# Kernel optimization log

Hardware: AMD Instinct MI355X
Metric: run time of the kernel (lower is better)

The kernel has to match this reference:

```python
import jax, jax.numpy as jnp
import numpy as np

N_HEAD = 16
SCALE = float(np.sqrt(1024 // N_HEAD))  # source multiplies by sqrt(head_dim) (faithful to bug)


def setup_inputs() -> dict:
    key = jax.random.key(0)
    ks = jax.random.split(key, 4)
    B, T, D = 4, 2048, 1024
    std = 1.0 / np.sqrt(D)
    return {
        "x": jax.random.normal(ks[0], (B, T, D), dtype=jnp.float32),
        "Wq": jax.random.normal(ks[1], (D, D), dtype=jnp.float32) * std,
        "bq": jnp.zeros((D,), dtype=jnp.float32),
        "Wk": jax.random.normal(ks[2], (D, D), dtype=jnp.float32) * std,
        "bk": jnp.zeros((D,), dtype=jnp.float32),
        "Wv": jax.random.normal(ks[3], (D, D), dtype=jnp.float32) * std,
        "bv": jnp.zeros((D,), dtype=jnp.float32),
    }


def reference(x, Wq, bq, Wk, bk, Wv, bv):
    B, T, D = x.shape
    H = N_HEAD
    hd = D // H
    # linear projections (torch Linear: x @ W^T + b)
    q = x @ Wq.T + bq
    k = x @ Wk.T + bk
    v = x @ Wv.T + bv
    # [B, H, T, hd]
    q = q.reshape(B, T, H, hd).transpose(0, 2, 1, 3)
    k = k.reshape(B, T, H, hd).transpose(0, 2, 1, 3)
    v = v.reshape(B, T, H, hd).transpose(0, 2, 1, 3)
    # scores [B, H, T, T]; note: source MULTIPLIES by sqrt(head_dim)
    att = jnp.einsum("bhqd,bhkd->bhqk", q, k) * SCALE
    causal = jnp.tril(jnp.ones((T, T), dtype=bool))
    att = jnp.where(causal, att, -jnp.inf)
    att = jax.nn.softmax(att, axis=-1)
    y = jnp.einsum("bhqk,bhkd->bhqd", att, v)
    return y.transpose(0, 2, 1, 3).reshape(B, T, D)
```

## Files before the change

kernel.cpp:

```cpp
#include <hip/hip_runtime.h>
#include <math.h>

#define TSEQ   2048
#define NBATCH 4
#define NHEAD  16
#define HDIM   64
#define DMODEL 1024
#define MROWS  (NBATCH * TSEQ)
#define QSCALE 11.541560327111707f

typedef float f32x4  __attribute__((ext_vector_type(4)));
typedef short bf16x8 __attribute__((ext_vector_type(8)));
typedef _Float16 f16x8 __attribute__((ext_vector_type(8)));

static __device__ __forceinline__ short f2bf(float f) {
    union { float f; unsigned u; } a; a.f = f;
    unsigned r = a.u + 0x7FFFu + ((a.u >> 16) & 1u);
    return (short)(r >> 16);
}
static __device__ __forceinline__ float bf2f(short s) {
    union { unsigned u; float f; } a; a.u = ((unsigned)(unsigned short)s) << 16;
    return a.f;
}
static __device__ __forceinline__ unsigned pkh(float a, float b) {
    union { _Float16 h[2]; unsigned u; } z;
    z.h[0] = (_Float16)a; z.h[1] = (_Float16)b;
    return z.u;
}

static __device__ __forceinline__ void async_copy16(void* lds, const void* g) {
    __builtin_amdgcn_global_load_lds(
        (const __attribute__((address_space(1))) void*)g,
        (__attribute__((address_space(3))) void*)lds, 16, 0, 0);
}

#define X_F4 (MROWS * DMODEL / 4)
#define W_F4 (DMODEL * DMODEL / 4)
__global__ __launch_bounds__(256) void split_all(
    const float* __restrict__ x,
    const float* __restrict__ wq, const float* __restrict__ wk,
    const float* __restrict__ wv,
    short* __restrict__ Xhi, short* __restrict__ Xlo,
    short* __restrict__ Whi, short* __restrict__ Wlo)
{
    int gid = blockIdx.x * 256 + threadIdx.x;
    const float* src; short* dh; short* dl; int off;
    if (gid < X_F4) {
        src = x; dh = Xhi; dl = Xlo; off = gid;
    } else {
        int r = gid - X_F4;
        int z = r >> 18;
        off = r & (W_F4 - 1);
        src = (z == 0) ? wq : (z == 1) ? wk : wv;
        dh = Whi + (size_t)z * DMODEL * DMODEL;
        dl = Wlo + (size_t)z * DMODEL * DMODEL;
    }
    float4 v = ((const float4*)src)[off];
    float f[4] = {v.x, v.y, v.z, v.w};
    short h[4], l[4];
    #pragma unroll
    for (int c = 0; c < 4; c++) {
        h[c] = f2bf(f[c]);
        l[c] = f2bf(f[c] - bf2f(h[c]));
    }
    *(float2*)(dh + (size_t)off * 4) = *(const float2*)h;
    *(float2*)(dl + (size_t)off * 4) = *(const float2*)l;
}

__global__ __launch_bounds__(256, 2) void qkv_gemm_mfma(
    const short* __restrict__ Xhi, const short* __restrict__ Xlo,
    const short* __restrict__ Wh3, const short* __restrict__ Wl3,
    const float* __restrict__ bq, const float* __restrict__ bk,
    const float* __restrict__ bv,
    short* __restrict__ Qhi, short* __restrict__ Qlo,
    short* __restrict__ Khi, short* __restrict__ Klo,
    _Float16* __restrict__ VgT)
{
    const int z = blockIdx.z;
    const bool dolo = (z != 2);
    const short* Wh = Wh3 + (size_t)z * DMODEL * DMODEL;
    const short* Wl = Wl3 + (size_t)z * DMODEL * DMODEL;
    const float* bias = (z == 0) ? bq : (z == 1) ? bk : bv;

    __shared__ __align__(16) short Ah[128 * 32];
    __shared__ __align__(16) short Al[128 * 32];
    __shared__ __align__(16) short Bh[128 * 32];
    __shared__ __align__(16) short Bl[128 * 32];

    const int tid  = threadIdx.x;
    const int w    = tid >> 6;
    const int lane = tid & 63;
    const int t    = lane & 15;
    const int quad = lane >> 4;
    const int wm   = w >> 1, wn = w & 1;

    const int orig = blockIdx.x + (blockIdx.y << 3);
    const int nw   = (orig & 7) * 64 + (orig >> 3);
    const int bm   = (nw >> 3) * 128;
    const int bn   = (nw & 7) * 128;

    const int r_local = lane >> 2;
    const int kq      = (lane & 3) ^ ((r_local >> 1) & 3);
    const int row0    = w * 32 + r_local;
    const int slotq   = (quad ^ ((t >> 1) & 3)) * 8;

    f32x4 acc[4][4];
    #pragma unroll
    for (int i = 0; i < 4; i++)
        #pragma unroll
        for (int j = 0; j < 4; j++) acc[i][j] = (f32x4){0.f, 0.f, 0.f, 0.f};

    for (int k0 = 0; k0 < DMODEL; k0 += 32) {
        __syncthreads();
        #pragma unroll
        for (int i = 0; i < 2; i++) {
            int row = row0 + i * 16;
            size_t ga = (size_t)(bm + row) * DMODEL + k0 + kq * 8;
            size_t gb = (size_t)(bn + row) * DMODEL + k0 + kq * 8;
            int ldst = (w * 32 + i * 16) * 32;
            async_copy16(&Ah[ldst], Xhi + ga);
            async_copy16(&Bh[ldst], Wh + gb);
            if (dolo) {
                async_copy16(&Al[ldst], Xlo + ga);
                async_copy16(&Bl[ldst], Wl + gb);
            }
        }
        __syncthreads();

        bf16x8 ah[4], al[4], bh[4], bl[4];
        #pragma unroll
        for (int mt = 0; mt < 4; mt++) {
            int off = (wm * 64 + mt * 16 + t) * 32 + slotq;
            ah[mt] = *(const bf16x8*)&Ah[off];
            if (dolo) al[mt] = *(const bf16x8*)&Al[off];
        }
        #pragma unroll
        for (int nt = 0; nt < 4; nt++) {
            int off = (wn * 64 + nt * 16 + t) * 32 + slotq;
            bh[nt] = *(const bf16x8*)&Bh[off];
            if (dolo) bl[nt] = *(const bf16x8*)&Bl[off];
        }
        #pragma unroll
        for (int mt = 0; mt < 4; mt++)
            #pragma unroll
            for (int nt = 0; nt < 4; nt++) {
                if (dolo) {
                    acc[mt][nt] = __builtin_amdgcn_mfma_f32_16x16x32_bf16(
                        al[mt], bh[nt], acc[mt][nt], 0, 0, 0);
                    acc[mt][nt] = __builtin_amdgcn_mfma_f32_16x16x32_bf16(
                        ah[mt], bl[nt], acc[mt][nt], 0, 0, 0);
                }
                acc[mt][nt] = __builtin_amdgcn_mfma_f32_16x16x32_bf16(
                    ah[mt], bh[nt], acc[mt][nt], 0, 0, 0);
            }
    }

    const float scale = (z == 0) ? QSCALE : 1.0f;
    const int n_base = bn + wn * 64;
    const int h_head = n_base >> 6;
    float bvs[4];
    #pragma unroll
    for (int nt = 0; nt < 4; nt++)
        bvs[nt] = bias[n_base + nt * 16 + t];

    #pragma unroll
    for (int mt = 0; mt < 4; mt++) {
        #pragma unroll
        for (int r = 0; r < 4; r++) {
            int m  = bm + wm * 64 + mt * 16 + quad * 4 + r;
            int b_ = m >> 11;
            int t_ = m & 2047;
            #pragma unroll
            for (int nt = 0; nt < 4; nt++) {
                int d = nt * 16 + t;
                float v = (acc[mt][nt][r] + bvs[nt]) * scale;
                if (z == 2) {
                    size_t idx = ((size_t)(b_ * NHEAD + h_head) * HDIM + d) * TSEQ + t_;
                    VgT[idx] = (_Float16)v;
                } else {
                    size_t idx = (((size_t)(b_ * NHEAD + h_head) * TSEQ + t_) << 6) + d;
                    short hb = f2bf(v);
                    short lb = f2bf(v - bf2f(hb));
                    if (z == 0) { Qhi[idx] = hb; Qlo[idx] = lb; }
                    else        { Khi[idx] = hb; Klo[idx] = lb; }
                }
            }
        }
    }
}

__global__ __launch_bounds__(256, 3) void attn_fwd(
    const short* __restrict__ Qhi, const short* __restrict__ Qlo,
    const short* __restrict__ Khi, const short* __restrict__ Klo,
    const _Float16* __restrict__ VgT,
    float* __restrict__ out)
{
    __shared__ __align__(16) short    Kh_lds[2][64 * 64];
    __shared__ __align__(16) short    Kl_lds[2][64 * 64];
    __shared__ __align__(16) _Float16 Vt_lds[2][64 * 64];

    const int tid  = threadIdx.x;

    const int l    = blockIdx.x;
    const int xcd  = l & 7;
    const int idx  = l >> 3;
    const int bh   = xcd * 8 + (idx & 7);
    const int qb   = 15 - (idx >> 3);

    const int b    = bh >> 4, h = bh & 15;
    const int w    = tid >> 6;
    const int lane = tid & 63;
    const int t    = lane & 15;
    const int quad = lane >> 4;

    const int rl      = w * 8 + (lane >> 3);
    const int chsw    = (lane & 7) ^ ((lane >> 3) & 7);
    const int ld_off  = (w * 8) * 64;

    const size_t kbase = (size_t)bh * TSEQ;
    const size_t vbase = (size_t)bh * HDIM;

    const int rs0 = ((0 * 4 + quad) ^ (t & 7)) * 8;
    const int rs1 = ((1 * 4 + quad) ^ (t & 7)) * 8;
    const int qsw = ((quad & 1) << 1) | (quad >> 1);
    const int rp0 = ((0 * 4 + qsw) ^ (t & 7)) * 8;
    const int rp1 = ((1 * 4 + qsw) ^ (t & 7)) * 8;
    const bool hi4 = (quad & 1);

    f16x8 ones;
    #pragma unroll
    for (int i = 0; i < 8; i++) ones[i] = (_Float16)1.0f;

    auto stage = [&](int kt, int bf) {
        #pragma unroll
        for (int i = 0; i < 2; i++) {
            int row = i * 32 + rl;
            const short* gk = Khi + (kbase + kt * 64 + row) * 64 + chsw * 8;
            async_copy16(&Kh_lds[bf][(i * 32) * 64 + ld_off], gk);
            const short* gl = Klo + (kbase + kt * 64 + row) * 64 + chsw * 8;
            async_copy16(&Kl_lds[bf][(i * 32) * 64 + ld_off], gl);
            const _Float16* gv = VgT + (vbase + row) * TSEQ + kt * 64 + chsw * 8;
            async_copy16(&Vt_lds[bf][(i * 32) * 64 + ld_off], gv);
        }
    };

    bf16x8 qh[2][2], ql[2][2];
    #pragma unroll
    for (int mt = 0; mt < 2; mt++) {
        size_t qrow = kbase + qb * 128 + w * 32 + mt * 16 + t;
        #pragma unroll
        for (int dh = 0; dh < 2; dh++) {
            qh[mt][dh] = *(const bf16x8*)(Qhi + qrow * 64 + dh * 32 + quad * 8);
            ql[mt][dh] = *(const bf16x8*)(Qlo + qrow * 64 + dh * 32 + quad * 8);
        }
    }

    f32x4 O[2][4], Ol[2];
    #pragma unroll
    for (int mt = 0; mt < 2; mt++) {
        Ol[mt] = (f32x4){0.f, 0.f, 0.f, 0.f};
        #pragma unroll
        for (int j = 0; j < 4; j++) O[mt][j] = (f32x4){0.f, 0.f, 0.f, 0.f};
    }
    float m_st[2];
    m_st[0] = -1e30f; m_st[1] = -1e30f;

    const int npair = qb + 1;

    #pragma unroll 1
    for (int p = 0; p < npair; p++) {
        __syncthreads();
        stage(2 * p, 0);
        stage(2 * p + 1, 1);
        __syncthreads();

        #pragma unroll
        for (int mt = 0; mt < 2; mt++) {
            f32x4 S[8];
            __builtin_amdgcn_s_setprio(1);
            #pragma unroll
            for (int c8 = 0; c8 < 8; c8++) {
                S[c8] = (f32x4){0.f, 0.f, 0.f, 0.f};
                const int bf = c8 >> 2;
                const int rowoff = ((c8 & 3) * 16 + t) * 64;
                {
                    bf16x8 kh = *(const bf16x8*)&Kh_lds[bf][rowoff + rs0];
                    bf16x8 kl = *(const bf16x8*)&Kl_lds[bf][rowoff + rs0];
                    S[c8] = __builtin_amdgcn_mfma_f32_16x16x32_bf16(kh, ql[mt][0], S[c8], 0, 0, 0);
                    S[c8] = __builtin_amdgcn_mfma_f32_16x16x32_bf16(kl, qh[mt][0], S[c8], 0, 0, 0);
                    S[c8] = __builtin_amdgcn_mfma_f32_16x16x32_bf16(kh, qh[mt][0], S[c8], 0, 0, 0);
                }
                {
                    bf16x8 kh = *(const bf16x8*)&Kh_lds[bf][rowoff + rs1];
                    bf16x8 kl = *(const bf16x8*)&Kl_lds[bf][rowoff + rs1];
                    S[c8] = __builtin_amdgcn_mfma_f32_16x16x32_bf16(kh, ql[mt][1], S[c8], 0, 0, 0);
                    S[c8] = __builtin_amdgcn_mfma_f32_16x16x32_bf16(kl, qh[mt][1], S[c8], 0, 0, 0);
                    S[c8] = __builtin_amdgcn_mfma_f32_16x16x32_bf16(kh, qh[mt][1], S[c8], 0, 0, 0);
                }
            }
            __builtin_amdgcn_s_setprio(0);

            if (p == qb) {
                const int qloc = w * 32 + mt * 16 + t;
                #pragma unroll
                for (int c8 = 0; c8 < 8; c8++) {
                    int kp = c8 * 16 + quad * 4;
                    #pragma unroll
                    for (int r = 0; r < 4; r++)
                        if (kp + r > qloc) S[c8][r] = -1e30f;
                }
            }

            float mx = S[0][0];
            #pragma unroll
            for (int c8 = 0; c8 < 8; c8++)
                #pragma unroll
                for (int r = 0; r < 4; r++)
                    mx = fmaxf(mx, S[c8][r]);
            mx = fmaxf(mx, __shfl_xor(mx, 16));
            mx = fmaxf(mx, __shfl_xor(mx, 32));

            bool need = mx > m_st[mt] + 8.0f;
            if (__ballot(need)) {
                float mn = fmaxf(m_st[mt], mx);
                float al = exp2f(m_st[mt] - mn);
                m_st[mt] = mn;
                #pragma unroll
                for (int r = 0; r < 4; r++) {
                    float a = __shfl(al, (lane & 48) + quad * 4 + r);
                    Ol[mt][r] *= a;
                    #pragma unroll
                    for (int ct2 = 0; ct2 < 4; ct2++) O[mt][ct2][r] *= a;
                }
            }

            #pragma unroll
            for (int c8 = 0; c8 < 8; c8++)
                #pragma unroll
                for (int r = 0; r < 4; r++)
                    S[c8][r] = exp2f(S[c8][r] - m_st[mt]);

            unsigned P2[8][2];
            #pragma unroll
            for (int c8 = 0; c8 < 8; c8++) {
                P2[c8][0] = pkh(S[c8][0], S[c8][1]);
                P2[c8][1] = pkh(S[c8][2], S[c8][3]);
            }

            unsigned FR[4][4];
            #pragma unroll
            for (int tau = 0; tau < 4; tau++) {
                #pragma unroll
                for (int rp = 0; rp < 2; rp++) {
                    unsigned X  = P2[2 * tau][rp];
                    unsigned Y  = P2[2 * tau + 1][rp];
                    unsigned Xs = (unsigned)__shfl_xor((int)X, 16);
                    unsigned Ys = (unsigned)__shfl_xor((int)Y, 16);
                    FR[tau][rp]     = hi4 ? Ys : X;
                    FR[tau][2 + rp] = hi4 ? Y  : Xs;
                }
            }

            #pragma unroll
            for (int tau = 0; tau < 4; tau++) {
                union { unsigned u[4]; f16x8 v; } pu;
                pu.u[0] = FR[tau][0]; pu.u[1] = FR[tau][1];
                pu.u[2] = FR[tau][2]; pu.u[3] = FR[tau][3];
                f16x8 pf = pu.v;
                const int bf  = tau >> 1;
                const int rsP = (tau & 1) ? rp1 : rp0;
                __builtin_amdgcn_s_setprio(1);
                #pragma unroll
                for (int ct2 = 0; ct2 < 4; ct2++) {
                    f16x8 v = *(const f16x8*)&Vt_lds[bf][(ct2 * 16 + t) * 64 + rsP];
                    O[mt][ct2] = __builtin_amdgcn_mfma_f32_16x16x32_f16(pf, v, O[mt][ct2], 0, 0, 0);
                }
                Ol[mt] = __builtin_amdgcn_mfma_f32_16x16x32_f16(pf, ones, Ol[mt], 0, 0, 0);
                __builtin_amdgcn_s_setprio(0);
            }
        }
    }

    #pragma unroll
    for (int mt = 0; mt < 2; mt++) {
        float* ob = out + ((size_t)b * TSEQ + qb * 128 + w * 32 + mt * 16 + quad * 4) * DMODEL
                  + h * 64;
        #pragma unroll
        for (int r = 0; r < 4; r++) {
            float inv = 1.0f / Ol[mt][r];
            #pragma unroll
            for (int ct2 = 0; ct2 < 4; ct2++)
                ob[(size_t)r * DMODEL + ct2 * 16 + t] = O[mt][ct2][r] * inv;
        }
    }
}

extern "C" void kernel_launch(void* const* d_in, const int* in_sizes, int n_in,
                              void* d_out, int out_size, void* d_ws, size_t ws_size,
                              hipStream_t stream)
{
    const float* x  = (const float*)d_in[0];
    const float* Wq = (const float*)d_in[1];
    const float* bq = (const float*)d_in[2];
    const float* Wk = (const float*)d_in[3];
    const float* bk = (const float*)d_in[4];
    const float* Wv = (const float*)d_in[5];
    const float* bv = (const float*)d_in[6];

    const size_t TEN = (size_t)MROWS * DMODEL;
    const size_t WEN = (size_t)DMODEL * DMODEL;
    short* Xhi = (short*)d_ws;
    short* Xlo = Xhi + TEN;
    short* Whi = Xlo + TEN;
    short* Wlo = Whi + 3 * WEN;
    short* Qhi = Wlo + 3 * WEN;
    short* Qlo = Qhi + TEN;
    short* Khi = Qlo + TEN;
    short* Klo = Khi + TEN;
    _Float16* VgT = (_Float16*)(Klo + TEN);
    float* out = (float*)d_out;

    int nsplit = (X_F4 + 3 * W_F4) / 256;
    split_all<<<nsplit, 256, 0, stream>>>(x, Wq, Wk, Wv, Xhi, Xlo, Whi, Wlo);

    dim3 gg(DMODEL / 128, MROWS / 128, 3);
    qkv_gemm_mfma<<<gg, 256, 0, stream>>>(Xhi, Xlo, Whi, Wlo, bq, bk, bv,
                                          Qhi, Qlo, Khi, Klo, VgT);

    attn_fwd<<<1024, 256, 0, stream>>>(Qhi, Qlo, Khi, Klo, VgT, out);
}
```

Baseline: 335.9 us.

## Switch split-precision QKV and QK^T from bf16 hi/lo to fp16 hi/residual

Replaces the bf16 hi/lo splitting with fp16 plus an fp16 residual throughout. The weights are now kept only as a single fp16 copy, so the Q/K projections drop from three MFMAs per tile to two and from four LDS stages to three. The attention score path keeps three MFMAs but now uses fp16 instead of bf16 operands. This cuts GEMM work and memory traffic for weights and X-lo, at the cost of fp16 range and overflow risk and less accuracy from dropping the weight low term.

```diff
diff --git a/kernel.cpp b/kernel.cpp
--- a/kernel.cpp
+++ b/kernel.cpp
@@ -10,18 +10,8 @@
 #define QSCALE 11.541560327111707f
 
 typedef float f32x4  __attribute__((ext_vector_type(4)));
-typedef short bf16x8 __attribute__((ext_vector_type(8)));
 typedef _Float16 f16x8 __attribute__((ext_vector_type(8)));
 
-static __device__ __forceinline__ short f2bf(float f) {
-    union { float f; unsigned u; } a; a.f = f;
-    unsigned r = a.u + 0x7FFFu + ((a.u >> 16) & 1u);
-    return (short)(r >> 16);
-}
-static __device__ __forceinline__ float bf2f(short s) {
-    union { unsigned u; float f; } a; a.u = ((unsigned)(unsigned short)s) << 16;
-    return a.f;
-}
 static __device__ __forceinline__ unsigned pkh(float a, float b) {
     union { _Float16 h[2]; unsigned u; } z;
     z.h[0] = (_Float16)a; z.h[1] = (_Float16)b;
@@ -36,56 +26,54 @@
 
 #define X_F4 (MROWS * DMODEL / 4)
 #define W_F4 (DMODEL * DMODEL / 4)
-__global__ __launch_bounds__(256) void split_all(
+__global__ __launch_bounds__(256) void cast_all(
     const float* __restrict__ x,
     const float* __restrict__ wq, const float* __restrict__ wk,
     const float* __restrict__ wv,
-    short* __restrict__ Xhi, short* __restrict__ Xlo,
-    short* __restrict__ Whi, short* __restrict__ Wlo)
+    _Float16* __restrict__ X16, _Float16* __restrict__ Xr,
+    _Float16* __restrict__ Wf)
 {
     int gid = blockIdx.x * 256 + threadIdx.x;
-    const float* src; short* dh; short* dl; int off;
     if (gid < X_F4) {
-        src = x; dh = Xhi; dl = Xlo; off = gid;
+        float4 v = ((const float4*)x)[gid];
+        float f[4] = {v.x, v.y, v.z, v.w};
+        _Float16 h[4], r[4];
+        #pragma unroll
+        for (int c = 0; c < 4; c++) {
+            h[c] = (_Float16)f[c];
+            r[c] = (_Float16)(f[c] - (float)h[c]);
+        }
+        *(float2*)(X16 + (size_t)gid * 4) = *(const float2*)h;
+        *(float2*)(Xr  + (size_t)gid * 4) = *(const float2*)r;
     } else {
-        int r = gid - X_F4;
-        int z = r >> 18;
-        off = r & (W_F4 - 1);
-        src = (z == 0) ? wq : (z == 1) ? wk : wv;
-        dh = Whi + (size_t)z * DMODEL * DMODEL;
-        dl = Wlo + (size_t)z * DMODEL * DMODEL;
-    }
-    float4 v = ((const float4*)src)[off];
-    float f[4] = {v.x, v.y, v.z, v.w};
-    short h[4], l[4];
-    #pragma unroll
-    for (int c = 0; c < 4; c++) {
-        h[c] = f2bf(f[c]);
-        l[c] = f2bf(f[c] - bf2f(h[c]));
-    }
-    *(float2*)(dh + (size_t)off * 4) = *(const float2*)h;
-    *(float2*)(dl + (size_t)off * 4) = *(const float2*)l;
+        int rr = gid - X_F4;
+        int z = rr >> 18;
+        int off = rr & (W_F4 - 1);
+        const float* src = (z == 0) ? wq : (z == 1) ? wk : wv;
+        _Float16* dst = Wf + (size_t)z * DMODEL * DMODEL;
+        float4 v = ((const float4*)src)[off];
+        _Float16 h[4] = {(_Float16)v.x, (_Float16)v.y, (_Float16)v.z, (_Float16)v.w};
+        *(float2*)(dst + (size_t)off * 4) = *(const float2*)h;
+    }
 }
 
 __global__ __launch_bounds__(256, 2) void qkv_gemm_mfma(
-    const short* __restrict__ Xhi, const short* __restrict__ Xlo,
-    const short* __restrict__ Wh3, const short* __restrict__ Wl3,
+    const _Float16* __restrict__ X16, const _Float16* __restrict__ Xr,
+    const _Float16* __restrict__ Wf3,
     const float* __restrict__ bq, const float* __restrict__ bk,
     const float* __restrict__ bv,
-    short* __restrict__ Qhi, short* __restrict__ Qlo,
-    short* __restrict__ Khi, short* __restrict__ Klo,
+    _Float16* __restrict__ Qh, _Float16* __restrict__ Qr,
+    _Float16* __restrict__ Kh, _Float16* __restrict__ Kr,
     _Float16* __restrict__ VgT)
 {
     const int z = blockIdx.z;
-    const bool dolo = (z != 2);
-    const short* Wh = Wh3 + (size_t)z * DMODEL * DMODEL;
-    const short* Wl = Wl3 + (size_t)z * DMODEL * DMODEL;
+    const bool dor = (z != 2);
+    const _Float16* W = Wf3 + (size_t)z * DMODEL * DMODEL;
     const float* bias = (z == 0) ? bq : (z == 1) ? bk : bv;
 
-    __shared__ __align__(16) short Ah[128 * 32];
-    __shared__ __align__(16) short Al[128 * 32];
-    __shared__ __align__(16) short Bh[128 * 32];
-    __shared__ __align__(16) short Bl[128 * 32];
+    __shared__ __align__(16) _Float16 Ah[128 * 32];
+    __shared__ __align__(16) _Float16 Ar[128 * 32];
+    __shared__ __align__(16) _Float16 Bh[128 * 32];
 
     const int tid  = threadIdx.x;
     const int w    = tid >> 6;
@@ -118,39 +106,32 @@
             size_t ga = (size_t)(bm + row) * DMODEL + k0 + kq * 8;
             size_t gb = (size_t)(bn + row) * DMODEL + k0 + kq * 8;
             int ldst = (w * 32 + i * 16) * 32;
-            async_copy16(&Ah[ldst], Xhi + ga);
-            async_copy16(&Bh[ldst], Wh + gb);
-            if (dolo) {
-                async_copy16(&Al[ldst], Xlo + ga);
-                async_copy16(&Bl[ldst], Wl + gb);
-            }
+            async_copy16(&Ah[ldst], X16 + ga);
+            async_copy16(&Bh[ldst], W + gb);
+            if (dor) async_copy16(&Ar[ldst], Xr + ga);
         }
         __syncthreads();
 
-        bf16x8 ah[4], al[4], bh[4], bl[4];
+        f16x8 ah[4], ar[4], bh[4];
         #pragma unroll
         for (int mt = 0; mt < 4; mt++) {
             int off = (wm * 64 + mt * 16 + t) * 32 + slotq;
-            ah[mt] = *(const bf16x8*)&Ah[off];
-            if (dolo) al[mt] = *(const bf16x8*)&Al[off];
+            ah[mt] = *(const f16x8*)&Ah[off];
+            if (dor) ar[mt] = *(const f16x8*)&Ar[off];
         }
         #pragma unroll
         for (int nt = 0; nt < 4; nt++) {
             int off = (wn * 64 + nt * 16 + t) * 32 + slotq;
-            bh[nt] = *(const bf16x8*)&Bh[off];
-            if (dolo) bl[nt] = *(const bf16x8*)&Bl[off];
+            bh[nt] = *(const f16x8*)&Bh[off];
         }
         #pragma unroll
         for (int mt = 0; mt < 4; mt++)
             #pragma unroll
             for (int nt = 0; nt < 4; nt++) {
-                if (dolo) {
-                    acc[mt][nt] = __builtin_amdgcn_mfma_f32_16x16x32_bf16(
-                        al[mt], bh[nt], acc[mt][nt], 0, 0, 0);
-                    acc[mt][nt] = __builtin_amdgcn_mfma_f32_16x16x32_bf16(
-                        ah[mt], bl[nt], acc[mt][nt], 0, 0, 0);
-                }
-                acc[mt][nt] = __builtin_amdgcn_mfma_f32_16x16x32_bf16(
+                if (dor)
+                    acc[mt][nt] = __builtin_amdgcn_mfma_f32_16x16x32_f16(
+                        ar[mt], bh[nt], acc[mt][nt], 0, 0, 0);
+                acc[mt][nt] = __builtin_amdgcn_mfma_f32_16x16x32_f16(
                     ah[mt], bh[nt], acc[mt][nt], 0, 0, 0);
             }
     }
@@ -179,10 +160,10 @@
                     VgT[idx] = (_Float16)v;
                 } else {
                     size_t idx = (((size_t)(b_ * NHEAD + h_head) * TSEQ + t_) << 6) + d;
-                    short hb = f2bf(v);
-                    short lb = f2bf(v - bf2f(hb));
-                    if (z == 0) { Qhi[idx] = hb; Qlo[idx] = lb; }
-                    else        { Khi[idx] = hb; Klo[idx] = lb; }
+                    _Float16 hb = (_Float16)v;
+                    _Float16 rb = (_Float16)(v - (float)hb);
+                    if (z == 0) { Qh[idx] = hb; Qr[idx] = rb; }
+                    else        { Kh[idx] = hb; Kr[idx] = rb; }
                 }
             }
         }
@@ -190,13 +171,13 @@
 }
 
 __global__ __launch_bounds__(256, 3) void attn_fwd(
-    const short* __restrict__ Qhi, const short* __restrict__ Qlo,
-    const short* __restrict__ Khi, const short* __restrict__ Klo,
+    const _Float16* __restrict__ Qh, const _Float16* __restrict__ Qr,
+    const _Float16* __restrict__ Kh, const _Float16* __restrict__ Kr,
     const _Float16* __restrict__ VgT,
     float* __restrict__ out)
 {
-    __shared__ __align__(16) short    Kh_lds[2][64 * 64];
-    __shared__ __align__(16) short    Kl_lds[2][64 * 64];
+    __shared__ __align__(16) _Float16 Kh_lds[2][64 * 64];
+    __shared__ __align__(16) _Float16 Kr_lds[2][64 * 64];
     __shared__ __align__(16) _Float16 Vt_lds[2][64 * 64];
 
     const int tid  = threadIdx.x;
@@ -235,23 +216,23 @@
         #pragma unroll
         for (int i = 0; i < 2; i++) {
             int row = i * 32 + rl;
-            const short* gk = Khi + (kbase + kt * 64 + row) * 64 + chsw * 8;
+            const _Float16* gk = Kh + (kbase + kt * 64 + row) * 64 + chsw * 8;
             async_copy16(&Kh_lds[bf][(i * 32) * 64 + ld_off], gk);
-            const short* gl = Klo + (kbase + kt * 64 + row) * 64 + chsw * 8;
-            async_copy16(&Kl_lds[bf][(i * 32) * 64 + ld_off], gl);
+            const _Float16* gr = Kr + (kbase + kt * 64 + row) * 64 + chsw * 8;
+            async_copy16(&Kr_lds[bf][(i * 32) * 64 + ld_off], gr);
             const _Float16* gv = VgT + (vbase + row) * TSEQ + kt * 64 + chsw * 8;
             async_copy16(&Vt_lds[bf][(i * 32) * 64 + ld_off], gv);
         }
     };
 
-    bf16x8 qh[2][2], ql[2][2];
+    f16x8 qh[2][2], qr[2][2];
     #pragma unroll
     for (int mt = 0; mt < 2; mt++) {
         size_t qrow = kbase + qb * 128 + w * 32 + mt * 16 + t;
         #pragma unroll
         for (int dh = 0; dh < 2; dh++) {
-            qh[mt][dh] = *(const bf16x8*)(Qhi + qrow * 64 + dh * 32 + quad * 8);
-            ql[mt][dh] = *(const bf16x8*)(Qlo + qrow * 64 + dh * 32 + quad * 8);
+            qh[mt][dh] = *(const f16x8*)(Qh + qrow * 64 + dh * 32 + quad * 8);
+            qr[mt][dh] = *(const f16x8*)(Qr + qrow * 64 + dh * 32 + quad * 8);
         }
     }
 
@@ -284,18 +265,18 @@
                 const int bf = c8 >> 2;
                 const int rowoff = ((c8 & 3) * 16 + t) * 64;
                 {
-                    bf16x8 kh = *(const bf16x8*)&Kh_lds[bf][rowoff + rs0];
-                    bf16x8 kl = *(const bf16x8*)&Kl_lds[bf][rowoff + rs0];
-                    S[c8] = __builtin_amdgcn_mfma_f32_16x16x32_bf16(kh, ql[mt][0], S[c8], 0, 0, 0);
-                    S[c8] = __builtin_amdgcn_mfma_f32_16x16x32_bf16(kl, qh[mt][0], S[c8], 0, 0, 0);
-                    S[c8] = __builtin_amdgcn_mfma_f32_16x16x32_bf16(kh, qh[mt][0], S[c8], 0, 0, 0);
+                    f16x8 kh = *(const f16x8*)&Kh_lds[bf][rowoff + rs0];
+                    f16x8 kr = *(const f16x8*)&Kr_lds[bf][rowoff + rs0];
+                    S[c8] = __builtin_amdgcn_mfma_f32_16x16x32_f16(kh, qr[mt][0], S[c8], 0, 0, 0);
+                    S[c8] = __builtin_amdgcn_mfma_f32_16x16x32_f16(kr, qh[mt][0], S[c8], 0, 0, 0);
+                    S[c8] = __builtin_amdgcn_mfma_f32_16x16x32_f16(kh, qh[mt][0], S[c8], 0, 0, 0);
                 }
                 {
-                    bf16x8 kh = *(const bf16x8*)&Kh_lds[bf][rowoff + rs1];
-                    bf16x8 kl = *(const bf16x8*)&Kl_lds[bf][rowoff + rs1];
-                    S[c8] = __builtin_amdgcn_mfma_f32_16x16x32_bf16(kh, ql[mt][1], S[c8], 0, 0, 0);
-                    S[c8] = __builtin_amdgcn_mfma_f32_16x16x32_bf16(kl, qh[mt][1], S[c8], 0, 0, 0);
-                    S[c8] = __builtin_amdgcn_mfma_f32_16x16x32_bf16(kh, qh[mt][1], S[c8], 0, 0, 0);
+                    f16x8 kh = *(const f16x8*)&Kh_lds[bf][rowoff + rs1];
+                    f16x8 kr = *(const f16x8*)&Kr_lds[bf][rowoff + rs1];
+                    S[c8] = __builtin_amdgcn_mfma_f32_16x16x32_f16(kh, qr[mt][1], S[c8], 0, 0, 0);
+                    S[c8] = __builtin_amdgcn_mfma_f32_16x16x32_f16(kr, qh[mt][1], S[c8], 0, 0, 0);
+                    S[c8] = __builtin_amdgcn_mfma_f32_16x16x32_f16(kh, qh[mt][1], S[c8], 0, 0, 0);
                 }
             }
             __builtin_amdgcn_s_setprio(0);
@@ -409,23 +390,22 @@
 
     const size_t TEN = (size_t)MROWS * DMODEL;
     const size_t WEN = (size_t)DMODEL * DMODEL;
-    short* Xhi = (short*)d_ws;
-    short* Xlo = Xhi + TEN;
-    short* Whi = Xlo + TEN;
-    short* Wlo = Whi + 3 * WEN;
-    short* Qhi = Wlo + 3 * WEN;
-    short* Qlo = Qhi + TEN;
-    short* Khi = Qlo + TEN;
-    short* Klo = Khi + TEN;
-    _Float16* VgT = (_Float16*)(Klo + TEN);
+    _Float16* X16 = (_Float16*)d_ws;
+    _Float16* Xr  = X16 + TEN;
+    _Float16* Wf  = Xr + TEN;
+    _Float16* Qh  = Wf + 3 * WEN;
+    _Float16* Qr  = Qh + TEN;
+    _Float16* Kh  = Qr + TEN;
+    _Float16* Kr  = Kh + TEN;
+    _Float16* VgT = Kr + TEN;
     float* out = (float*)d_out;
 
-    int nsplit = (X_F4 + 3 * W_F4) / 256;
-    split_all<<<nsplit, 256, 0, stream>>>(x, Wq, Wk, Wv, Xhi, Xlo, Whi, Wlo);
+    int ncast = (X_F4 + 3 * W_F4) / 256;
+    cast_all<<<ncast, 256, 0, stream>>>(x, Wq, Wk, Wv, X16, Xr, Wf);
 
     dim3 gg(DMODEL / 128, MROWS / 128, 3);
-    qkv_gemm_mfma<<<gg, 256, 0, stream>>>(Xhi, Xlo, Whi, Wlo, bq, bk, bv,
-                                          Qhi, Qlo, Khi, Klo, VgT);
-
-    attn_fwd<<<1024, 256, 0, stream>>>(Qhi, Qlo, Khi, Klo, VgT, out);
-}
+    qkv_gemm_mfma<<<gg, 256, 0, stream>>>(X16, Xr, Wf, bq, bk, bv,
+                                          Qh, Qr, Kh, Kr, VgT);
+
+    attn_fwd<<<1024, 256, 0, stream>>>(Qh, Qr, Kh, Kr, VgT, out);
+}
```

After: 305.6 us. 1.1x faster.
